# Optimization experiments

Hardware: AMD Instinct MI355X
Metric: run time of the kernel (lower is better)

Reference implementation:

```python
import jax, jax.numpy as jnp
import numpy as np
import math

N_HEAD = 16
V_HEAD = 32   # v_head_dim
NOPE = 32     # nope_head_dim
ROPE_D = 64   # rope_head_dim
KEEP = 256    # num_tokens_to_keep
EPS = 1e-6


def _freqs(T, dim=ROPE_D, theta=10000.0):
    f = 1.0 / (theta ** (jnp.arange(0, dim, 2, dtype=jnp.float32) / dim))
    t = jnp.arange(T, dtype=jnp.float32)
    a = jnp.outer(t, f)  # [T, dim//2]
    return jnp.cos(a), jnp.sin(a)


def _rope(x, cos, sin):
    # x: [B,H,S,D]; half-split rotation as in apply_rope
    S = x.shape[-2]
    c = cos[:S][None, None]
    s = sin[:S][None, None]
    x1, x2 = jnp.split(x, 2, axis=-1)
    return jnp.concatenate([x1 * c - x2 * s, x1 * s + x2 * c], axis=-1)


def _rms(x, g, eps=EPS):
    return x * jax.lax.rsqrt(jnp.mean(x * x, axis=-1, keepdims=True) + eps) * g


def _attn(q, k, v, causal):
    scale = 1.0 / math.sqrt(q.shape[-1])
    s = jnp.einsum('bhqd,bhkd->bhqk', q, k) * scale
    if causal:
        Tq, Tk = s.shape[-2], s.shape[-1]
        mask = jnp.tril(jnp.ones((Tq, Tk), dtype=bool))
        s = jnp.where(mask, s, jnp.finfo(s.dtype).min)
    return jnp.einsum('bhqk,bhkd->bhqd', jax.nn.softmax(s, axis=-1), v)


def _forward(x, w_cq, g_qnorm, w_dq_nope, w_dq_rope, w_ckv, g_kvnorm,
             w_dk_nope, w_dv, w_krope, w_imp, w_selk, w_selv,
             w_wink, w_winv, w_gate, w_proj):
    B, T, C = x.shape
    cos, sin = _freqs(T)

    # --- MLA query path ---
    nq = _rms(x @ w_cq, g_qnorm)                                  # [B,T,96]
    q_nope = (nq @ w_dq_nope).reshape(B, T, N_HEAD, NOPE).transpose(0, 2, 1, 3)
    q_rope = (nq @ w_dq_rope).reshape(B, T, N_HEAD, ROPE_D).transpose(0, 2, 1, 3)
    q_rope = _rope(q_rope, cos, sin)
    q = jnp.concatenate([q_nope, q_rope], axis=-1)                # [B,H,T,96]

    # --- branch gate ---
    gate = jax.nn.softmax((x @ w_gate).mean(axis=1), axis=-1)     # [B,3]

    # --- branch 1: MLA-compressed full KV ---
    ckv = _rms(x @ w_ckv, g_kvnorm)                               # [B,T,32]
    k_nope = (ckv @ w_dk_nope).reshape(B, T, N_HEAD, NOPE).transpose(0, 2, 1, 3)
    v1 = (ckv @ w_dv).reshape(B, T, N_HEAD, V_HEAD).transpose(0, 2, 1, 3)
    k_rope = (x @ w_krope).reshape(B, T, 1, ROPE_D).transpose(0, 2, 1, 3) / N_HEAD
    k_rope = _rope(k_rope, cos, sin)
    k1 = jnp.concatenate(
        [k_nope, jnp.broadcast_to(k_rope, (B, N_HEAD, T, ROPE_D))], axis=-1)

    # --- branch 2: top-k selected tokens ---
    scores = (x @ w_imp)[..., 0]                                  # [B,T]
    _, idx = jax.lax.top_k(scores, KEEP)
    idx = jnp.sort(idx, axis=1)
    sel = jnp.take_along_axis(x, idx[:, :, None], axis=1)         # [B,S,C]
    ks = (sel @ w_selk).reshape(B, KEEP, N_HEAD, NOPE + ROPE_D).transpose(0, 2, 1, 3)
    vs = (sel @ w_selv).reshape(B, KEEP, N_HEAD, V_HEAD).transpose(0, 2, 1, 3)
    ks = jnp.concatenate([ks[..., :NOPE], _rope(ks[..., NOPE:], cos, sin)], axis=-1)

    # --- branch 3: sliding window (training mode -> full x) ---
    kw = (x @ w_wink).reshape(B, T, N_HEAD, NOPE + ROPE_D).transpose(0, 2, 1, 3)
    vw = (x @ w_winv).reshape(B, T, N_HEAD, V_HEAD).transpose(0, 2, 1, 3)
    kw = jnp.concatenate([kw[..., :NOPE], _rope(kw[..., NOPE:], cos, sin)], axis=-1)

    a1 = _attn(q, k1, v1, causal=True)
    a2 = _attn(q, ks, vs, causal=False)
    a3 = _attn(q, kw, vw, causal=True)

    g = gate[:, :, None, None, None]
    out = g[:, 0] * a1 + g[:, 1] * a2 + g[:, 2] * a3              # [B,H,T,Vd]
    out = out.transpose(0, 2, 1, 3).reshape(B, T, N_HEAD * V_HEAD)
    return out @ w_proj                                           # [B,T,C]


def setup_inputs() -> dict:
    key = jax.random.key(0)
    ks = jax.random.split(key, 20)
    B, T, C = 2, 1024, 1024
    q_lora, kv_lora = 96, 32
    std = 0.02
    def w(k, shape):
        return jax.random.normal(k, shape, dtype=jnp.float32) * std
    return {
        'x': jax.random.normal(ks[0], (B, T, C), dtype=jnp.float32),
        'w_cq': w(ks[1], (C, q_lora)),
        'g_qnorm': jnp.ones((q_lora,), jnp.float32),
        'w_dq_nope': w(ks[2], (q_lora, N_HEAD * NOPE)),
        'w_dq_rope': w(ks[3], (q_lora, N_HEAD * ROPE_D)),
        'w_ckv': w(ks[4], (C, kv_lora)),
        'g_kvnorm': jnp.ones((kv_lora,), jnp.float32),
        'w_dk_nope': w(ks[5], (kv_lora, N_HEAD * NOPE)),
        'w_dv': w(ks[6], (kv_lora, N_HEAD * V_HEAD)),
        'w_krope': w(ks[7], (C, ROPE_D)),
        'w_imp': w(ks[8], (C, 1)),
        'w_selk': w(ks[9], (C, N_HEAD * (NOPE + ROPE_D))),
        'w_selv': w(ks[10], (C, N_HEAD * V_HEAD)),
        'w_wink': w(ks[11], (C, N_HEAD * (NOPE + ROPE_D))),
        'w_winv': w(ks[12], (C, N_HEAD * V_HEAD)),
        'w_gate': w(ks[13], (C, 3)),
        'w_proj': w(ks[14], (N_HEAD * V_HEAD, C)),
    }


def reference(x, w_cq, g_qnorm, w_dq_nope, w_dq_rope, w_ckv, g_kvnorm,
              w_dk_nope, w_dv, w_krope, w_imp, w_selk, w_selv,
              w_wink, w_winv, w_gate, w_proj):
    return _forward(x, w_cq, g_qnorm, w_dq_nope, w_dq_rope, w_ckv, g_kvnorm,
                    w_dk_nope, w_dv, w_krope, w_imp, w_selk, w_selv,
                    w_wink, w_winv, w_gate, w_proj)
```

## Files before the change

### kernel.cpp

```cpp
#include <hip/hip_runtime.h>
#include <math.h>

#define T_SEQ   1024
#define BATCH   2
#define CDIM    1024
#define NHEAD   16
#define VHEAD   32
#define KEEP    256
#define HEAD_D  96
#define SCALE_ATTN 0.1020620726159658f

#define BQ   64
#define BKT  64
#define SK   100
#define SPT  66
#define SPV  36

#define GBK 16
#define SA  132

#define XWW    2244
#define C_CQ   0
#define C_CKV  96
#define C_KRO  128
#define C_WINK 192
#define C_WINV 1728
#define C_IMP  2240
#define C_GATE 2241

#define QKVW   2560
#define C_QN   0
#define C_QR   512
#define C_KN   1536
#define C_V1   2048

#define SKW  2048

__global__ __launch_bounds__(256) void gemm128(const float* __restrict__ A,
                                               const float* __restrict__ B,
                                               float* __restrict__ C,
                                               int M, int N, int K,
                                               int lda, int ldb, int ldc,
                                               int kchunk) {
    __shared__ float As[GBK][SA];
    __shared__ float Bs[GBK][SA];
    int t = threadIdx.x;
    int tx = t & 15, ty = t >> 4;
    int row0 = blockIdx.y * 128, col0 = blockIdx.x * 128;
    int kb = blockIdx.z * kchunk;
    int ke = min(K, kb + kchunk);
    float acc[8][8] = {};

    for (int k0 = kb; k0 < ke; k0 += GBK) {
#pragma unroll
        for (int r = 0; r < 2; r++) {
            int idx = t + 256 * r;
            int row = idx >> 2, k4 = idx & 3;
            int gr = row0 + row;
            float4 v = make_float4(0.f, 0.f, 0.f, 0.f);
            if (gr < M) v = *(const float4*)&A[(size_t)gr * lda + k0 + k4 * 4];
            As[k4 * 4 + 0][row] = v.x;
            As[k4 * 4 + 1][row] = v.y;
            As[k4 * 4 + 2][row] = v.z;
            As[k4 * 4 + 3][row] = v.w;
        }
#pragma unroll
        for (int r = 0; r < 2; r++) {
            int idx = t + 256 * r;
            int kk = idx >> 5, n4 = idx & 31;
            int gc = col0 + n4 * 4;
            float4 v = make_float4(0.f, 0.f, 0.f, 0.f);
            if (gc + 3 < N) {
                v = *(const float4*)&B[(size_t)(k0 + kk) * ldb + gc];
            } else if (gc < N) {
                const float* bp = &B[(size_t)(k0 + kk) * ldb];
                float tmp[4] = {0.f, 0.f, 0.f, 0.f};
                for (int j = 0; j < 4 && gc + j < N; j++) tmp[j] = bp[gc + j];
                v = make_float4(tmp[0], tmp[1], tmp[2], tmp[3]);
            }
            *(float4*)&Bs[kk][n4 * 4] = v;
        }
        __syncthreads();
#pragma unroll
        for (int kk = 0; kk < GBK; kk++) {
            float4 a0 = *(float4*)&As[kk][ty * 4];
            float4 a1 = *(float4*)&As[kk][64 + ty * 4];
            float4 b0 = *(float4*)&Bs[kk][tx * 4];
            float4 b1 = *(float4*)&Bs[kk][64 + tx * 4];
            float av[8] = {a0.x, a0.y, a0.z, a0.w, a1.x, a1.y, a1.z, a1.w};
            float bv[8] = {b0.x, b0.y, b0.z, b0.w, b1.x, b1.y, b1.z, b1.w};
#pragma unroll
            for (int i = 0; i < 8; i++)
#pragma unroll
                for (int j = 0; j < 8; j++) acc[i][j] += av[i] * bv[j];
        }
        __syncthreads();
    }

    bool split = (gridDim.z > 1);
#pragma unroll
    for (int i = 0; i < 8; i++) {
        int gr = row0 + ((i < 4) ? (ty * 4 + i) : (64 + ty * 4 + (i - 4)));
        if (gr >= M) continue;
#pragma unroll
        for (int half = 0; half < 2; half++) {
            int gc = col0 + half * 64 + tx * 4;
            if (gc + 3 >= N) continue;
            float* cp = &C[(size_t)gr * ldc + gc];
            if (split) {
                atomicAdd(cp + 0, acc[i][half * 4 + 0]);
                atomicAdd(cp + 1, acc[i][half * 4 + 1]);
                atomicAdd(cp + 2, acc[i][half * 4 + 2]);
                atomicAdd(cp + 3, acc[i][half * 4 + 3]);
            } else {
                *(float4*)cp = make_float4(acc[i][half * 4 + 0], acc[i][half * 4 + 1],
                                           acc[i][half * 4 + 2], acc[i][half * 4 + 3]);
            }
        }
    }
}

__global__ void pack_xw(float* __restrict__ dst,
                        const float* __restrict__ cq, const float* __restrict__ ckv,
                        const float* __restrict__ kro, const float* __restrict__ wink,
                        const float* __restrict__ winv, const float* __restrict__ imp,
                        const float* __restrict__ gate) {
    int r = blockIdx.x;
    for (int c = threadIdx.x; c < XWW; c += blockDim.x) {
        float v;
        if      (c < C_CKV)  v = cq  [(size_t)r * 96   + c];
        else if (c < C_KRO)  v = ckv [(size_t)r * 32   + (c - C_CKV)];
        else if (c < C_WINK) v = kro [(size_t)r * 64   + (c - C_KRO)];
        else if (c < C_WINV) v = wink[(size_t)r * 1536 + (c - C_WINK)];
        else if (c < C_IMP)  v = winv[(size_t)r * 512  + (c - C_WINV)];
        else if (c < C_GATE) v = imp [(size_t)r * 1    + (c - C_IMP)];
        else                 v = gate[(size_t)r * 3    + (c - C_GATE)];
        dst[(size_t)r * XWW + c] = v;
    }
}

__global__ void pack_qkv(float* __restrict__ dst,
                         const float* __restrict__ dqn, const float* __restrict__ dqr,
                         const float* __restrict__ dkn, const float* __restrict__ dv) {
    int r = blockIdx.x;
    for (int c = threadIdx.x; c < QKVW; c += blockDim.x) {
        float v = 0.f;
        if (r < 96) {
            if (c < C_QR)      v = dqn[(size_t)r * 512 + c];
            else if (c < C_KN) v = dqr[(size_t)r * 1024 + (c - C_QR)];
        } else {
            if (c >= C_KN && c < C_V1) v = dkn[(size_t)(r - 96) * 512 + (c - C_KN)];
            else if (c >= C_V1)        v = dv [(size_t)(r - 96) * 512 + (c - C_V1)];
        }
        dst[(size_t)r * QKVW + c] = v;
    }
}

__global__ void pack2(float* __restrict__ dst,
                      const float* __restrict__ s0, int w0,
                      const float* __restrict__ s1, int w1) {
    int W = w0 + w1;
    int r = blockIdx.x;
    for (int c = threadIdx.x; c < W; c += blockDim.x) {
        float v = (c < w0) ? s0[(size_t)r * w0 + c] : s1[(size_t)r * w1 + (c - w0)];
        dst[(size_t)r * W + c] = v;
    }
}

__global__ void rms_rows(float* __restrict__ buf, const float* __restrict__ g,
                         int D, int stride) {
    int row = blockIdx.x;
    int lane = threadIdx.x;
    float* rp = buf + (size_t)row * stride;
    float ss = 0.f;
    for (int d = lane; d < D; d += 64) {
        float v = rp[d];
        ss += v * v;
    }
    for (int off = 32; off; off >>= 1) ss += __shfl_xor(ss, off, 64);
    float r = rsqrtf(ss / (float)D + 1e-6f);
    for (int d = lane; d < D; d += 64) rp[d] *= r * g[d];
}

__global__ void rope_inplace(float* __restrict__ buf, int nrows, int rstride,
                             int nheads, int hstride, int roff, int posmod,
                             float scale) {
    int total = nrows * nheads * 32;
    for (int it = blockIdx.x * blockDim.x + threadIdx.x; it < total;
         it += gridDim.x * blockDim.x) {
        int i = it & 31;
        int hr = it >> 5;
        int h = hr % nheads;
        int row = hr / nheads;
        int pos = row % posmod;
        float expo = (float)i * (1.0f / 32.0f);
        float f = 1.0f / powf(10000.0f, expo);
        float a = (float)pos * f;
        float s, c;
        sincosf(a, &s, &c);
        size_t base = (size_t)row * rstride + (size_t)h * hstride + roff;
        float v1 = buf[base + i], v2 = buf[base + 32 + i];
        buf[base + i]      = (v1 * c - v2 * s) * scale;
        buf[base + 32 + i] = (v1 * s + v2 * c) * scale;
    }
}

__global__ void gate_from_cols(const float* __restrict__ xw, float* __restrict__ gate) {
    int b = blockIdx.x;
    int t = threadIdx.x;
    __shared__ float red[3][4];
    float g0 = 0.f, g1 = 0.f, g2 = 0.f;
    for (int r = t; r < T_SEQ; r += 256) {
        const float* p = &xw[((size_t)b * T_SEQ + r) * XWW + C_GATE];
        g0 += p[0]; g1 += p[1]; g2 += p[2];
    }
    for (int off = 32; off; off >>= 1) {
        g0 += __shfl_xor(g0, off, 64);
        g1 += __shfl_xor(g1, off, 64);
        g2 += __shfl_xor(g2, off, 64);
    }
    int w = t >> 6;
    if ((t & 63) == 0) { red[0][w] = g0; red[1][w] = g1; red[2][w] = g2; }
    __syncthreads();
    if (t == 0) {
        float v0 = (red[0][0] + red[0][1] + red[0][2] + red[0][3]) / (float)T_SEQ;
        float v1 = (red[1][0] + red[1][1] + red[1][2] + red[1][3]) / (float)T_SEQ;
        float v2 = (red[2][0] + red[2][1] + red[2][2] + red[2][3]) / (float)T_SEQ;
        float m = fmaxf(v0, fmaxf(v1, v2));
        float e0 = expf(v0 - m), e1 = expf(v1 - m), e2 = expf(v2 - m);
        float s = e0 + e1 + e2;
        gate[b * 3 + 0] = e0 / s;
        gate[b * 3 + 1] = e1 / s;
        gate[b * 3 + 2] = e2 / s;
    }
}

__global__ void topk_kernel(const float* __restrict__ base, int stride, int col,
                            int* __restrict__ idx) {
    int b = blockIdx.x;
    __shared__ float s[1024];
    __shared__ int ps[1024];
    int t = threadIdx.x;
    s[t] = base[((size_t)b * T_SEQ + t) * stride + col];
    __syncthreads();
    float mine = s[t];
    int rank = 0;
    for (int j = 0; j < 1024; j++) {
        float v = s[j];
        rank += (v > mine) || (v == mine && j < t);
    }
    int selv = (rank < KEEP) ? 1 : 0;
    ps[t] = selv;
    __syncthreads();
    for (int off = 1; off < 1024; off <<= 1) {
        int add = (t >= off) ? ps[t - off] : 0;
        __syncthreads();
        ps[t] += add;
        __syncthreads();
    }
    if (selv) idx[b * KEEP + ps[t] - 1] = t;
}

__global__ void gather_sel(const float* __restrict__ x, const int* __restrict__ idx,
                           float* __restrict__ sel) {
    for (size_t i = (size_t)blockIdx.x * blockDim.x + threadIdx.x;
         i < (size_t)BATCH * KEEP * CDIM; i += (size_t)gridDim.x * blockDim.x) {
        int c = (int)(i & (CDIM - 1));
        int r = (int)((i >> 10) & (KEEP - 1));
        int b = (int)(i >> 18);
        sel[i] = x[((size_t)b * T_SEQ + idx[b * KEEP + r]) * CDIM + c];
    }
}

__global__ __launch_bounds__(512, 4) void flash_fused(
    const float* __restrict__ qkv, const float* __restrict__ xw,
    const float* __restrict__ skv, const float* __restrict__ gate,
    float* __restrict__ out) {
    __shared__ float Qs[BQ * SK];
    __shared__ float Ks[BKT * SK];
    __shared__ float Vs[BKT * SPV];
    __shared__ float Pt[BKT * SPT];
    __shared__ float mrow[BQ], lrow[BQ], arow[BQ], mtil[BQ];

    int b = blockIdx.z, h = blockIdx.y;
    int qt = blockIdx.x;
    if (b == 1) qt = (gridDim.x - 1) - qt;
    int q0 = qt * BQ;
    int t = threadIdx.x;
    int tq = t >> 4, tk = t & 15;
    int qg = t >> 4, dg = t & 15;

    for (int i = t; i < BQ * 24; i += 512) {
        int row = i / 24, d4 = i % 24;
        size_t rq = (size_t)b * T_SEQ + q0 + row;
        float4 v;
        if (d4 < 8) v = *(const float4*)&qkv[rq * QKVW + C_QN + h * 32 + d4 * 4];
        else        v = *(const float4*)&qkv[rq * QKVW + C_QR + h * 64 + (d4 - 8) * 4];
        *(float4*)&Qs[row * SK + d4 * 4] = v;
    }

    float comb[2][2] = {};
    for (int phase = 0; phase < 3; phase++) {
        bool causal = (phase != 1);
        int ntiles = causal ? (qt + 1) : (KEEP / BKT);
        float o00 = 0.f, o01 = 0.f, o10 = 0.f, o11 = 0.f;
        __syncthreads();
        if (t < BQ) { mrow[t] = -1e30f; lrow[t] = 0.f; }

        for (int kt = 0; kt < ntiles; kt++) {
            int j0 = kt * BKT;
            __syncthreads();

            for (int i = t; i < BKT * 24; i += 512) {
                int row = i / 24, d4 = i % 24;
                int j = j0 + row;
                float4 v;
                if (phase == 0) {
                    size_t rk = (size_t)b * T_SEQ + j;
                    if (d4 < 8) v = *(const float4*)&qkv[rk * QKVW + C_KN + h * 32 + d4 * 4];
                    else        v = *(const float4*)&xw[rk * XWW + C_KRO + (d4 - 8) * 4];
                } else if (phase == 1) {
                    v = *(const float4*)&skv[((size_t)b * KEEP + j) * SKW + h * 96 + d4 * 4];
                } else {
                    v = *(const float4*)&xw[((size_t)b * T_SEQ + j) * XWW + C_WINK + h * 96 + d4 * 4];
                }
                *(float4*)&Ks[row * SK + d4 * 4] = v;
            }
            for (int i = t; i < BKT * 8; i += 512) {
                int row = i >> 3, d4 = i & 7;
                int j = j0 + row;
                float4 v;
                if (phase == 0)      v = *(const float4*)&qkv[((size_t)b * T_SEQ + j) * QKVW + C_V1 + h * 32 + d4 * 4];
                else if (phase == 1) v = *(const float4*)&skv[((size_t)b * KEEP  + j) * SKW + 1536 + h * 32 + d4 * 4];
                else                 v = *(const float4*)&xw[((size_t)b * T_SEQ + j) * XWW + C_WINV + h * 32 + d4 * 4];
                *(float4*)&Vs[row * SPV + d4 * 4] = v;
            }
            __syncthreads();

            float s[2][4] = {};
#pragma unroll 6
            for (int d = 0; d < HEAD_D; d += 4) {
                float4 qa = *(float4*)&Qs[(2 * tq)     * SK + d];
                float4 qb = *(float4*)&Qs[(2 * tq + 1) * SK + d];
#pragma unroll
                for (int j = 0; j < 4; j++) {
                    float4 kv = *(float4*)&Ks[(16 * j + tk) * SK + d];
                    s[0][j] += qa.x * kv.x + qa.y * kv.y + qa.z * kv.z + qa.w * kv.w;
                    s[1][j] += qb.x * kv.x + qb.y * kv.y + qb.z * kv.z + qb.w * kv.w;
                }
            }
#pragma unroll
            for (int i = 0; i < 2; i++)
#pragma unroll
                for (int j = 0; j < 4; j++) {
                    int qq = q0 + 2 * tq + i;
                    int kk = j0 + 16 * j + tk;
                    float sv = s[i][j] * SCALE_ATTN;
                    if (causal && kk > qq) sv = -1e30f;
                    Pt[(16 * j + tk) * SPT + (2 * tq + i)] = sv;
                }
            __syncthreads();

            {
                int q = t >> 3, sub = t & 7;
                float mt = -1e30f;
#pragma unroll
                for (int i2 = 0; i2 < 8; i2++)
                    mt = fmaxf(mt, Pt[(sub * 8 + i2) * SPT + q]);
                mt = fmaxf(mt, __shfl_xor(mt, 1, 64));
                mt = fmaxf(mt, __shfl_xor(mt, 2, 64));
                mt = fmaxf(mt, __shfl_xor(mt, 4, 64));
                if (sub == 0) mtil[q] = mt;
            }
            __syncthreads();
            if (t < BQ) {
                float mnew = fmaxf(mrow[t], mtil[t]);
                arow[t] = __expf(mrow[t] - mnew);
                mrow[t] = mnew;
            }
            __syncthreads();
            {
                int q = t >> 3, sub = t & 7;
                float mnew = mrow[q];
                float psum = 0.f;
#pragma unroll
                for (int i2 = 0; i2 < 8; i2++) {
                    int kk = sub * 8 + i2;
                    float p = __expf(Pt[kk * SPT + q] - mnew);
                    Pt[kk * SPT + q] = p;
                    psum += p;
                }
                psum += __shfl_xor(psum, 1, 64);
                psum += __shfl_xor(psum, 2, 64);
                psum += __shfl_xor(psum, 4, 64);
                if (sub == 0) lrow[q] = lrow[q] * arow[q] + psum;
            }
            __syncthreads();

            {
                float a0 = arow[2 * qg], a1 = arow[2 * qg + 1];
                o00 *= a0; o01 *= a0; o10 *= a1; o11 *= a1;
#pragma unroll 8
                for (int kk = 0; kk < BKT; kk++) {
                    float2 pv = *(float2*)&Pt[kk * SPT + 2 * qg];
                    float2 vv = *(float2*)&Vs[kk * SPV + 2 * dg];
                    o00 += pv.x * vv.x; o01 += pv.x * vv.y;
                    o10 += pv.y * vv.x; o11 += pv.y * vv.y;
                }
            }
        }

        {
            float g = gate[b * 3 + phase];
            float i0 = g / lrow[2 * qg], i1 = g / lrow[2 * qg + 1];
            comb[0][0] += o00 * i0; comb[0][1] += o01 * i0;
            comb[1][0] += o10 * i1; comb[1][1] += o11 * i1;
        }
    }

    size_t r0 = ((size_t)b * T_SEQ + q0 + 2 * qg) * 512 + h * 32 + 2 * dg;
    out[r0]           = comb[0][0];
    out[r0 + 1]       = comb[0][1];
    out[r0 + 512]     = comb[1][0];
    out[r0 + 512 + 1] = comb[1][1];
}

extern "C" void kernel_launch(void* const* d_in, const int* in_sizes, int n_in,
                              void* d_out, int out_size, void* d_ws, size_t ws_size,
                              hipStream_t stream) {
    const float* x        = (const float*)d_in[0];
    const float* w_cq     = (const float*)d_in[1];
    const float* g_qnorm  = (const float*)d_in[2];
    const float* w_dqn    = (const float*)d_in[3];
    const float* w_dqr    = (const float*)d_in[4];
    const float* w_ckv    = (const float*)d_in[5];
    const float* g_kvnorm = (const float*)d_in[6];
    const float* w_dkn    = (const float*)d_in[7];
    const float* w_dv     = (const float*)d_in[8];
    const float* w_krope  = (const float*)d_in[9];
    const float* w_imp    = (const float*)d_in[10];
    const float* w_selk   = (const float*)d_in[11];
    const float* w_selv   = (const float*)d_in[12];
    const float* w_wink   = (const float*)d_in[13];
    const float* w_winv   = (const float*)d_in[14];
    const float* w_gate   = (const float*)d_in[15];
    const float* w_proj   = (const float*)d_in[16];
    float* out = (float*)d_out;

    const int BT = BATCH * T_SEQ;
    const int BS = BATCH * KEEP;

    float* ws = (float*)d_ws;
    size_t o = 0;
    float* XW     = ws + o; o += (size_t)BT * XWW;
    float* QKV    = ws + o; o += (size_t)BT * QKVW;
    float* skv    = ws + o; o += (size_t)BS * SKW;
    float* selb   = ws + o; o += (size_t)BS * CDIM;
    float* attn   = ws + o; o += (size_t)BT * 512;
    float* Bxw    = ws + o; o += (size_t)CDIM * XWW;
    float* Bqkv   = ws + o; o += (size_t)128 * QKVW;
    float* Bsel   = ws + o; o += (size_t)CDIM * SKW;
    float* gatef  = ws + o; o += 8;
    int*   idx    = (int*)(ws + o); o += 512;

    auto gemm = [&](const float* A, const float* Bm, float* C, int M, int N, int K,
                    int lda, int ldb, int ldc, int ksplit = 1) {
        int kchunk = (K / ksplit + GBK - 1) / GBK * GBK;
        dim3 grid((N + 127) / 128, (M + 127) / 128, ksplit);
        gemm128<<<grid, 256, 0, stream>>>(A, Bm, C, M, N, K, lda, ldb, ldc, kchunk);
    };

    hipMemsetAsync(skv, 0, (size_t)BS * SKW * sizeof(float), stream);
    hipMemsetAsync(out, 0, (size_t)BT * CDIM * sizeof(float), stream);

    pack_xw<<<1024, 256, 0, stream>>>(Bxw, w_cq, w_ckv, w_krope, w_wink, w_winv,
                                      w_imp, w_gate);
    pack_qkv<<<128, 256, 0, stream>>>(Bqkv, w_dqn, w_dqr, w_dkn, w_dv);
    pack2<<<1024, 256, 0, stream>>>(Bsel, w_selk, 1536, w_selv, 512);

    gemm(x, Bxw, XW, BT, XWW, CDIM, CDIM, XWW, XWW);

    rms_rows<<<BT, 64, 0, stream>>>(XW + C_CQ, g_qnorm, 96, XWW);
    rms_rows<<<BT, 64, 0, stream>>>(XW + C_CKV, g_kvnorm, 32, XWW);
    rope_inplace<<<256, 256, 0, stream>>>(XW, BT, XWW, 1, 0, C_KRO, T_SEQ, 1.0f / NHEAD);
    rope_inplace<<<2048, 256, 0, stream>>>(XW, BT, XWW, 16, 96, C_WINK + 32, T_SEQ, 1.0f);

    gate_from_cols<<<BATCH, 256, 0, stream>>>(XW, gatef);
    topk_kernel<<<BATCH, 1024, 0, stream>>>(XW, XWW, C_IMP, idx);
    gather_sel<<<2048, 256, 0, stream>>>(x, idx, selb);

    gemm(XW, Bqkv, QKV, BT, QKVW, 128, XWW, QKVW, QKVW);
    rope_inplace<<<2048, 256, 0, stream>>>(QKV, BT, QKVW, 16, 64, C_QR, T_SEQ, 1.0f);

    gemm(selb, Bsel, skv, BS, SKW, CDIM, CDIM, SKW, SKW, 4);
    rope_inplace<<<512, 256, 0, stream>>>(skv, BS, SKW, 16, 96, 32, KEEP, 1.0f);

    dim3 fgrid(T_SEQ / BQ, NHEAD, BATCH);
    flash_fused<<<fgrid, 512, 0, stream>>>(QKV, XW, skv, gatef, attn);

    gemm(attn, w_proj, out, BT, CDIM, 512, 512, CDIM, CDIM, 2);
}
```

Baseline: 1.001 ms.

## Keep online-softmax row statistics in registers with wavefront shuffles

Moves the per-row running max, rescale factor and row sum out of shared memory and into registers. Each 16-lane group that owns a query-row pair reduces its scores with xor shuffles. This drops the shared mrow/lrow/arow/mtil arrays, a separate pass that wrote raw scores to Pt and read them back, and several block-wide barriers per key tile. Only the exponentiated probabilities are now written to Pt for the P·V product. That step depends on lanes within one wavefront seeing each other's LDS writes without an explicit barrier, which relies on wavefront execution order rather than an explicit fence.

```diff
diff --git a/kernel.cpp b/kernel.cpp
--- a/kernel.cpp
+++ b/kernel.cpp
@@ -280,7 +280,6 @@
     __shared__ float Ks[BKT * SK];
     __shared__ float Vs[BKT * SPV];
     __shared__ float Pt[BKT * SPT];
-    __shared__ float mrow[BQ], lrow[BQ], arow[BQ], mtil[BQ];
 
     int b = blockIdx.z, h = blockIdx.y;
     int qt = blockIdx.x;
@@ -288,7 +287,6 @@
     int q0 = qt * BQ;
     int t = threadIdx.x;
     int tq = t >> 4, tk = t & 15;
-    int qg = t >> 4, dg = t & 15;
 
     for (int i = t; i < BQ * 24; i += 512) {
         int row = i / 24, d4 = i % 24;
@@ -299,13 +297,13 @@
         *(float4*)&Qs[row * SK + d4 * 4] = v;
     }
 
+    int qq0 = q0 + 2 * tq, qq1 = qq0 + 1;
     float comb[2][2] = {};
     for (int phase = 0; phase < 3; phase++) {
         bool causal = (phase != 1);
         int ntiles = causal ? (qt + 1) : (KEEP / BKT);
+        float m0 = -1e30f, m1 = -1e30f, l0 = 0.f, l1 = 0.f;
         float o00 = 0.f, o01 = 0.f, o10 = 0.f, o11 = 0.f;
-        __syncthreads();
-        if (t < BQ) { mrow[t] = -1e30f; lrow[t] = 0.f; }
 
         for (int kt = 0; kt < ntiles; kt++) {
             int j0 = kt * BKT;
@@ -337,7 +335,7 @@
             }
             __syncthreads();
 
-            float s[2][4] = {};
+            float s0[4] = {}, s1[4] = {};
 #pragma unroll 6
             for (int d = 0; d < HEAD_D; d += 4) {
                 float4 qa = *(float4*)&Qs[(2 * tq)     * SK + d];
@@ -345,80 +343,63 @@
 #pragma unroll
                 for (int j = 0; j < 4; j++) {
                     float4 kv = *(float4*)&Ks[(16 * j + tk) * SK + d];
-                    s[0][j] += qa.x * kv.x + qa.y * kv.y + qa.z * kv.z + qa.w * kv.w;
-                    s[1][j] += qb.x * kv.x + qb.y * kv.y + qb.z * kv.z + qb.w * kv.w;
+                    s0[j] += qa.x * kv.x + qa.y * kv.y + qa.z * kv.z + qa.w * kv.w;
+                    s1[j] += qb.x * kv.x + qb.y * kv.y + qb.z * kv.z + qb.w * kv.w;
                 }
             }
-#pragma unroll
-            for (int i = 0; i < 2; i++)
-#pragma unroll
-                for (int j = 0; j < 4; j++) {
-                    int qq = q0 + 2 * tq + i;
-                    int kk = j0 + 16 * j + tk;
-                    float sv = s[i][j] * SCALE_ATTN;
-                    if (causal && kk > qq) sv = -1e30f;
-                    Pt[(16 * j + tk) * SPT + (2 * tq + i)] = sv;
-                }
-            __syncthreads();
-
-            {
-                int q = t >> 3, sub = t & 7;
-                float mt = -1e30f;
-#pragma unroll
-                for (int i2 = 0; i2 < 8; i2++)
-                    mt = fmaxf(mt, Pt[(sub * 8 + i2) * SPT + q]);
-                mt = fmaxf(mt, __shfl_xor(mt, 1, 64));
-                mt = fmaxf(mt, __shfl_xor(mt, 2, 64));
-                mt = fmaxf(mt, __shfl_xor(mt, 4, 64));
-                if (sub == 0) mtil[q] = mt;
-            }
-            __syncthreads();
-            if (t < BQ) {
-                float mnew = fmaxf(mrow[t], mtil[t]);
-                arow[t] = __expf(mrow[t] - mnew);
-                mrow[t] = mnew;
-            }
-            __syncthreads();
-            {
-                int q = t >> 3, sub = t & 7;
-                float mnew = mrow[q];
-                float psum = 0.f;
-#pragma unroll
-                for (int i2 = 0; i2 < 8; i2++) {
-                    int kk = sub * 8 + i2;
-                    float p = __expf(Pt[kk * SPT + q] - mnew);
-                    Pt[kk * SPT + q] = p;
-                    psum += p;
-                }
-                psum += __shfl_xor(psum, 1, 64);
-                psum += __shfl_xor(psum, 2, 64);
-                psum += __shfl_xor(psum, 4, 64);
-                if (sub == 0) lrow[q] = lrow[q] * arow[q] + psum;
-            }
-            __syncthreads();
-
-            {
-                float a0 = arow[2 * qg], a1 = arow[2 * qg + 1];
-                o00 *= a0; o01 *= a0; o10 *= a1; o11 *= a1;
+            float mt0 = -1e30f, mt1 = -1e30f;
+#pragma unroll
+            for (int j = 0; j < 4; j++) {
+                int kk = j0 + 16 * j + tk;
+                s0[j] *= SCALE_ATTN;
+                s1[j] *= SCALE_ATTN;
+                if (causal && kk > qq0) s0[j] = -1e30f;
+                if (causal && kk > qq1) s1[j] = -1e30f;
+                mt0 = fmaxf(mt0, s0[j]);
+                mt1 = fmaxf(mt1, s1[j]);
+            }
+#pragma unroll
+            for (int off = 1; off <= 8; off <<= 1) {
+                mt0 = fmaxf(mt0, __shfl_xor(mt0, off, 64));
+                mt1 = fmaxf(mt1, __shfl_xor(mt1, off, 64));
+            }
+            float mn0 = fmaxf(m0, mt0), mn1 = fmaxf(m1, mt1);
+            float a0 = __expf(m0 - mn0), a1 = __expf(m1 - mn1);
+            m0 = mn0; m1 = mn1;
+
+            float rs0 = 0.f, rs1 = 0.f;
+#pragma unroll
+            for (int j = 0; j < 4; j++) {
+                float p0 = __expf(s0[j] - mn0);
+                float p1 = __expf(s1[j] - mn1);
+                rs0 += p0; rs1 += p1;
+                *(float2*)&Pt[(16 * j + tk) * SPT + 2 * tq] = make_float2(p0, p1);
+            }
+#pragma unroll
+            for (int off = 1; off <= 8; off <<= 1) {
+                rs0 += __shfl_xor(rs0, off, 64);
+                rs1 += __shfl_xor(rs1, off, 64);
+            }
+            l0 = l0 * a0 + rs0;
+            l1 = l1 * a1 + rs1;
+
+            o00 *= a0; o01 *= a0; o10 *= a1; o11 *= a1;
 #pragma unroll 8
-                for (int kk = 0; kk < BKT; kk++) {
-                    float2 pv = *(float2*)&Pt[kk * SPT + 2 * qg];
-                    float2 vv = *(float2*)&Vs[kk * SPV + 2 * dg];
-                    o00 += pv.x * vv.x; o01 += pv.x * vv.y;
-                    o10 += pv.y * vv.x; o11 += pv.y * vv.y;
-                }
-            }
-        }
-
-        {
-            float g = gate[b * 3 + phase];
-            float i0 = g / lrow[2 * qg], i1 = g / lrow[2 * qg + 1];
-            comb[0][0] += o00 * i0; comb[0][1] += o01 * i0;
-            comb[1][0] += o10 * i1; comb[1][1] += o11 * i1;
-        }
-    }
-
-    size_t r0 = ((size_t)b * T_SEQ + q0 + 2 * qg) * 512 + h * 32 + 2 * dg;
+            for (int kk = 0; kk < BKT; kk++) {
+                float2 pv = *(float2*)&Pt[kk * SPT + 2 * tq];
+                float2 vv = *(float2*)&Vs[kk * SPV + 2 * tk];
+                o00 += pv.x * vv.x; o01 += pv.x * vv.y;
+                o10 += pv.y * vv.x; o11 += pv.y * vv.y;
+            }
+        }
+
+        float g = gate[b * 3 + phase];
+        float i0 = g / l0, i1 = g / l1;
+        comb[0][0] += o00 * i0; comb[0][1] += o01 * i0;
+        comb[1][0] += o10 * i1; comb[1][1] += o11 * i1;
+    }
+
+    size_t r0 = ((size_t)b * T_SEQ + q0 + 2 * tq) * 512 + h * 32 + 2 * tk;
     out[r0]           = comb[0][0];
     out[r0 + 1]       = comb[0][1];
     out[r0 + 512]     = comb[1][0];
```

After: 978.7 us. -2.2%, faster.
